# Kernel tuning notes

Hardware: AMD Instinct MI355X
Metric: run time of the kernel (lower is better)

## Reference

```python
import jax, jax.numpy as jnp
import numpy as np

BATCH = 256
NUM_PIXELS = 4096
NUM_LATENT = 8192
NUM_STEPS = 50
STEP_SIZE = 0.1
SPARSE_MULT = 0.1
EPS = 1e-8


def setup_inputs() -> dict:
    key = jax.random.key(0)
    k1, k2 = jax.random.split(key)
    input_tensor = jax.random.normal(k1, (BATCH, NUM_PIXELS), dtype=jnp.float32)
    w = jax.random.normal(k2, (NUM_PIXELS, NUM_LATENT), dtype=jnp.float32)
    # l2-normalize each dictionary element (column over pixel dim), as in dp.l2_normalize_weights
    w = w / (jnp.linalg.norm(w, axis=0, keepdims=True) + EPS)
    return {"input_tensor": input_tensor, "w": w}


def _threshold(u):
    # soft threshold with rectify_a=True: a = max(u - lambda, 0)
    return jnp.where(u > SPARSE_MULT, u - SPARSE_MULT, jnp.zeros_like(u))


def reference(input_tensor, w):
    # excitatory drive b = x @ w, constant over inference steps  [B, L]
    excitatory = jnp.matmul(input_tensor, w)
    # inhibitory Gram matrix G = w^T w - I  [L, L]
    gram = jnp.matmul(w.T, w) - jnp.eye(NUM_LATENT, dtype=w.dtype)

    def body(u, _):
        a = _threshold(u)
        du = excitatory - jnp.matmul(a, gram) - u
        return u + STEP_SIZE * du, None

    u0 = jnp.zeros((input_tensor.shape[0], NUM_LATENT), dtype=input_tensor.dtype)
    u_final, _ = jax.lax.scan(body, u0, None, length=NUM_STEPS - 1)
    a_final = _threshold(u_final)
    # reconstruction = a @ w^T  [B, P]
    return jnp.matmul(a_final, w.T)
```

## Files before the change

### kernel.cpp

```cpp
#include <hip/hip_runtime.h>
#include <stdint.h>
#include <math.h>

#define B_DIM 256
#define P_DIM 4096
#define L_DIM 8192
#define NSTEPS 50
#define STEP 0.1f
#define LAM 0.1f
#define FP8_ITERS 40
#define GSCALE 64.0f
#define ASCALE 16.0f
#define INV_SCALE (1.0f / (64.0f * 16.0f))

typedef __attribute__((ext_vector_type(8))) short bf16x8;
typedef __attribute__((ext_vector_type(4))) float f32x4;
typedef __attribute__((ext_vector_type(2))) long lgx2;

__device__ __forceinline__ unsigned short f2bf(float f) {
    union { float f; uint32_t u; } x; x.f = f;
    uint32_t r = (x.u + 0x7FFF + ((x.u >> 16) & 1)) >> 16;
    return (unsigned short)r;
}
__device__ __forceinline__ float bf2f(unsigned short h) {
    union { uint32_t u; float f; } x; x.u = (uint32_t)h << 16; return x.f;
}


__global__ void cast_x_kernel(const float* __restrict__ in, unsigned short* __restrict__ out, int n) {
    int i = (blockIdx.x * blockDim.x + threadIdx.x) * 4;
    if (i < n) {
        float4 v = *(const float4*)&in[i];
        ushort4 o;
        o.x = f2bf(v.x); o.y = f2bf(v.y); o.z = f2bf(v.z); o.w = f2bf(v.w);
        *(ushort4*)&out[i] = o;
    }
}

__global__ void cast_transpose_w(const float* __restrict__ w,
                                 unsigned short* __restrict__ w_bf,
                                 unsigned short* __restrict__ wT_bf) {
    __shared__ float tile[32][33];
    int c0 = blockIdx.x * 32;
    int r0 = blockIdx.y * 32;
    int tx = threadIdx.x, ty = threadIdx.y;
#pragma unroll
    for (int i = ty; i < 32; i += 8) {
        float v = w[(size_t)(r0 + i) * L_DIM + c0 + tx];
        tile[i][tx] = v;
        w_bf[(size_t)(r0 + i) * L_DIM + c0 + tx] = f2bf(v);
    }
    __syncthreads();
#pragma unroll
    for (int i = ty; i < 32; i += 8) {
        wT_bf[(size_t)(c0 + i) * P_DIM + r0 + tx] = f2bf(tile[tx][i]);
    }
}

__global__ void quantize_G(const unsigned short* __restrict__ G, unsigned char* __restrict__ Gf) {
    size_t i = ((size_t)blockIdx.x * 256 + threadIdx.x) * 8;
    bf16x8 v = *(const bf16x8*)&G[i];
    float f[8];
#pragma unroll
    for (int j = 0; j < 8; ++j) f[j] = bf2f((unsigned short)v[j]) * GSCALE;
    int q0 = __builtin_amdgcn_cvt_pk_fp8_f32(f[0], f[1], 0, false);
    q0 = __builtin_amdgcn_cvt_pk_fp8_f32(f[2], f[3], q0, true);
    int q1 = __builtin_amdgcn_cvt_pk_fp8_f32(f[4], f[5], 0, false);
    q1 = __builtin_amdgcn_cvt_pk_fp8_f32(f[6], f[7], q1, true);
    const int r = (int)(i & 127);
    size_t dst = (i & ~(size_t)127) + (size_t)((((r >> 6) & 1) << 6) + (((r >> 3) & 3) << 4) + (((r >> 5) & 1) << 3));
    *(int2*)(Gf + dst) = make_int2(q0, q1);
}

template <int BM, int BN, int BK, int WMC, int WNC, int EPI, int MM, int NN, int KK, int MAP>
__global__ __launch_bounds__(WMC * WNC * 64)
void gemm_pipe(const unsigned short* __restrict__ A,
               const unsigned short* __restrict__ Bt,
               float* __restrict__ Cf,
               float* __restrict__ uvec,
               unsigned short* __restrict__ aout,
               unsigned char* __restrict__ afp8) {
    constexpr int NWAVES = WMC * WNC;
    constexpr int WM = BM / WMC, WN = BN / WNC;
    constexpr int MF = WM / 16, NF = WN / 16;
    constexpr int ACH = BM / (8 * NWAVES);
    constexpr int BCH = BN / (8 * NWAVES);
    constexpr int LPS = ACH + BCH;
    constexpr int NT = KK / BK;
    static_assert(BK == 64, "swizzle hardcoded for BK=64");
    static_assert(ACH * 8 * NWAVES == BM && BCH * 8 * NWAVES == BN, "stage geometry");
    static_assert(NT % 4 == 0 && NT >= 8, "pipeline geometry");

    __shared__ __align__(16) unsigned short As[4][BM * BK];
    __shared__ __align__(16) unsigned short Bs[4][BN * BK];

    const int tid = threadIdx.x;
    const int w = tid >> 6;
    const int l = tid & 63;
    const int wr = w / WNC, wc = w % WNC;

    const int id = blockIdx.x;
    int bx, by;
    if constexpr (MAP == 0) {
        constexpr int PPX = (NN / BN) / 8;
        static_assert(MM / BM == 4 && (NN / BN) % 8 == 0, "panel map geometry");
        bx = (id & 7) * PPX + ((id >> 3) >> 2);
        by = (id >> 3) & 3;
    } else {
        constexpr int GY = MM / BM;
        by = id % GY;
        bx = id / GY;
    }
    const int row0 = by * BM;
    const int col0 = bx * BN;

    const int lrow = l >> 3;
    const int lcol = (((l & 7) ^ lrow) * 8);

    const unsigned short* gA = A + (size_t)(row0 + lrow) * KK + lcol;
    const unsigned short* gB = Bt + (size_t)(col0 + lrow) * KK + lcol;

    auto stage = [&](int buf, int k0) {
#pragma unroll
        for (int i = 0; i < ACH; ++i) {
            const int chunk = i * NWAVES + w;
            __builtin_amdgcn_global_load_lds(
                (const __attribute__((address_space(1))) void*)(gA + (size_t)chunk * 8 * KK + k0),
                (__attribute__((address_space(3))) void*)(&As[buf][chunk * 512]), 16, 0, 0);
        }
#pragma unroll
        for (int i = 0; i < BCH; ++i) {
            const int chunk = i * NWAVES + w;
            __builtin_amdgcn_global_load_lds(
                (const __attribute__((address_space(1))) void*)(gB + (size_t)chunk * 8 * KK + k0),
                (__attribute__((address_space(3))) void*)(&Bs[buf][chunk * 512]), 16, 0, 0);
        }
    };

    f32x4 acc[MF][NF] = {};

    auto compute = [&](int buf) {
#pragma unroll
        for (int kk = 0; kk < BK; kk += 32) {
            const int kslot = (kk >> 3) + (l >> 4);
            bf16x8 af[MF], bfr[NF];
#pragma unroll
            for (int mf = 0; mf < MF; ++mf) {
                const int arow = wr * WM + mf * 16 + (l & 15);
                af[mf] = *(const bf16x8*)&As[buf][arow * BK + ((kslot ^ (arow & 7)) << 3)];
            }
#pragma unroll
            for (int nf = 0; nf < NF; ++nf) {
                const int brow = wc * WN + nf * 16 + (l & 15);
                bfr[nf] = *(const bf16x8*)&Bs[buf][brow * BK + ((kslot ^ (brow & 7)) << 3)];
            }
#pragma unroll
            for (int mf = 0; mf < MF; ++mf)
#pragma unroll
                for (int nf = 0; nf < NF; ++nf)
                    acc[mf][nf] = __builtin_amdgcn_mfma_f32_16x16x32_bf16(
                        af[mf], bfr[nf], acc[mf][nf], 0, 0, 0);
        }
    };

#define PH(BUF, TT, WAITN, DOSTG)                                            \
    asm volatile("s_waitcnt vmcnt(%0)" ::"i"(WAITN) : "memory");             \
    __builtin_amdgcn_s_barrier();                                            \
    asm volatile("" ::: "memory");                                           \
    if (DOSTG) stage((BUF + 3) & 3, ((TT) + 3) * BK);                        \
    compute(BUF);

    stage(0, 0);
    stage(1, BK);
    stage(2, 2 * BK);
#pragma unroll 1
    for (int t = 0; t < NT - 4; t += 4) {
        PH(0, t + 0, 2 * LPS, true)
        PH(1, t + 1, 2 * LPS, true)
        PH(2, t + 2, 2 * LPS, true)
        PH(3, t + 3, 2 * LPS, true)
    }
    PH(0, NT - 4, 2 * LPS, true)
    PH(1, NT - 3, 2 * LPS, false)
    PH(2, NT - 2, LPS, false)
    PH(3, NT - 1, 0, false)
#undef PH

    const int er = (l >> 4) * 4;
    const int ec = l & 15;
#pragma unroll
    for (int mf = 0; mf < MF; ++mf) {
#pragma unroll
        for (int nf = 0; nf < NF; ++nf) {
#pragma unroll
            for (int j = 0; j < 4; ++j) {
                int gr = row0 + wr * WM + mf * 16 + er + j;
                int gc = col0 + wc * WN + nf * 16 + ec;
                size_t idx = (size_t)gr * NN + gc;
                float v = acc[mf][nf][j];
                if constexpr (EPI == 1) {
                    Cf[idx] = v;
                    float u0 = STEP * v;
                    uvec[idx] = u0;
                    float a = (u0 > LAM) ? (u0 - LAM) : 0.0f;
                    aout[idx] = f2bf(a);
                    float a16 = a * ASCALE;
                    int q = __builtin_amdgcn_cvt_pk_fp8_f32(a16, a16, 0, false);
                    const int r = gc & 127;
                    size_t fd = (size_t)gr * L_DIM + (size_t)(gc & ~127) +
                                (size_t)((((r >> 6) & 1) << 6) + (((r >> 3) & 3) << 4) + (((r >> 5) & 1) << 3) + (r & 7));
                    afp8[fd] = (unsigned char)(q & 0xff);
                } else {
                    Cf[idx] = v;
                }
            }
        }
    }
}

__global__ __launch_bounds__(512, 2)
void gemm_gram_sym(const unsigned short* __restrict__ A,
                   unsigned short* __restrict__ G) {
    constexpr int BM = 256, BN = 256, BK = 64;
    constexpr int WMC = 2, WNC = 4, NWAVES = 8;
    constexpr int WM = 128, WN = 64, MF = 8, NF = 4;
    constexpr int ACH = 4, BCH = 4, LPS = 8;
    constexpr int NT = P_DIM / BK;

    __shared__ __align__(16) unsigned short sh[4 * 256 * 64];
#define ASB(buf) (sh + (buf) * (256 * 64))
#define BSB(buf) (sh + (2 + (buf)) * (256 * 64))

    const int tid = threadIdx.x;
    const int w = tid >> 6;
    const int l = tid & 63;
    const int wr = w / WNC, wc = w % WNC;

    const int id = blockIdx.x;
    const int i = (int)((65.0f - sqrtf(4225.0f - 8.0f * (float)id)) * 0.5f);
    const int cum = i * (65 - i) / 2;
    const int j = i + (id - cum);
    const int by = i, bx = j;
    const int row0 = by * BM;
    const int col0 = bx * BN;

    const int lrow = l >> 3;
    const int lcol = (((l & 7) ^ lrow) * 8);

    const unsigned short* gA = A + (size_t)(row0 + lrow) * P_DIM + lcol;
    const unsigned short* gB = A + (size_t)(col0 + lrow) * P_DIM + lcol;

    auto stage = [&](int buf, int t) {
        const int k0 = t * BK;
#pragma unroll
        for (int c = 0; c < ACH; ++c) {
            const int chunk = c * NWAVES + w;
            __builtin_amdgcn_global_load_lds(
                (const __attribute__((address_space(1))) void*)(gA + (size_t)chunk * 8 * P_DIM + k0),
                (__attribute__((address_space(3))) void*)(ASB(buf) + chunk * 512), 16, 0, 0);
        }
#pragma unroll
        for (int c = 0; c < BCH; ++c) {
            const int chunk = c * NWAVES + w;
            __builtin_amdgcn_global_load_lds(
                (const __attribute__((address_space(1))) void*)(gB + (size_t)chunk * 8 * P_DIM + k0),
                (__attribute__((address_space(3))) void*)(BSB(buf) + chunk * 512), 16, 0, 0);
        }
    };

    f32x4 acc[MF][NF] = {};

    auto compute = [&](int buf) {
#pragma unroll
        for (int kk = 0; kk < BK; kk += 32) {
            const int kslot = (kk >> 3) + (l >> 4);
            bf16x8 af[MF], bfr[NF];
#pragma unroll
            for (int mf = 0; mf < MF; ++mf) {
                const int arow = wr * WM + mf * 16 + (l & 15);
                af[mf] = *(const bf16x8*)&ASB(buf)[arow * BK + ((kslot ^ (arow & 7)) << 3)];
            }
#pragma unroll
            for (int nf = 0; nf < NF; ++nf) {
                const int brow = wc * WN + nf * 16 + (l & 15);
                bfr[nf] = *(const bf16x8*)&BSB(buf)[brow * BK + ((kslot ^ (brow & 7)) << 3)];
            }
#pragma unroll
            for (int mf = 0; mf < MF; ++mf)
#pragma unroll
                for (int nf = 0; nf < NF; ++nf)
                    acc[mf][nf] = __builtin_amdgcn_mfma_f32_16x16x32_bf16(
                        af[mf], bfr[nf], acc[mf][nf], 0, 0, 0);
        }
    };

#define PH2(BUF, WAITN, DOSTG, TT)                                           \
    asm volatile("s_waitcnt vmcnt(%0)" ::"i"(WAITN) : "memory");             \
    __builtin_amdgcn_s_barrier();                                            \
    asm volatile("" ::: "memory");                                           \
    compute(BUF);                                                            \
    __builtin_amdgcn_s_barrier();                                            \
    asm volatile("" ::: "memory");                                           \
    if (DOSTG) stage(BUF, (TT) + 2);

    stage(0, 0);
    stage(1, 1);
#pragma unroll 1
    for (int t = 0; t < NT - 2; t += 2) {
        PH2(0, LPS, true, t)
        PH2(1, LPS, true, t + 1)
    }
    PH2(0, LPS, false, 0)
    PH2(1, 0, false, 0)
#undef PH2

    const int er = (l >> 4) * 4;
    const int ec = l & 15;

#pragma unroll
    for (int mf = 0; mf < MF; ++mf)
#pragma unroll
        for (int nf = 0; nf < NF; ++nf)
#pragma unroll
            for (int jj = 0; jj < 4; ++jj) {
                int gr = row0 + wr * WM + mf * 16 + er + jj;
                int gc = col0 + wc * WN + nf * 16 + ec;
                float v = acc[mf][nf][jj];
                if (gr == gc) v -= 1.0f;
                G[(size_t)gr * L_DIM + gc] = f2bf(v);
            }

    if (by != bx) {
        unsigned short* T = sh;
#pragma unroll 1
        for (int p = 0; p < 2; ++p) {
            __syncthreads();
            if ((wc >> 1) == p) {
#pragma unroll
                for (int mf = 0; mf < MF; ++mf)
#pragma unroll
                    for (int nf = 0; nf < NF; ++nf)
#pragma unroll
                        for (int jj = 0; jj < 4; ++jj) {
                            const int gr_l = wr * WM + mf * 16 + er + jj;
                            const int gc_l = (wc & 1) * 64 + nf * 16 + ec;
                            T[gc_l * 256 + (gr_l ^ ((gc_l & 7) << 2))] = f2bf(acc[mf][nf][jj]);
                        }
            }
            __syncthreads();
            const int rr = tid >> 6;
            const int cc = (tid & 63) * 4;
#pragma unroll
            for (int s = 0; s < 16; ++s) {
                const int r = s * 8 + rr;
                uint2 val = *(const uint2*)&T[r * 256 + (cc ^ ((r & 7) << 2))];
                *(uint2*)&G[(size_t)(col0 + p * 128 + r) * L_DIM + row0 + cc] = val;
            }
        }
    }
#undef ASB
#undef BSB
}

template <int BM, int BN, int WMC, int WNC, int EPI, int KROW, int KLOOP, int MAP>
__global__ __launch_bounds__(WMC * WNC * 64, 2)
void gemm2(const unsigned short* __restrict__ A,
           const unsigned short* __restrict__ Bt,
           unsigned short* __restrict__ Obf) {
    constexpr int NWAVES = WMC * WNC;
    constexpr int WM = BM / WMC, WN = BN / WNC;
    constexpr int MF = WM / 16, NF = WN / 16;
    constexpr int ACH = BM / (8 * NWAVES);
    constexpr int BCH = BN / (8 * NWAVES);
    constexpr int LPS = ACH + BCH;
    constexpr int BK = 64;
    constexpr int NT = KLOOP / BK;
    static_assert(ACH * 8 * NWAVES == BM && BCH * 8 * NWAVES == BN, "stage geometry");
    static_assert(NT % 2 == 0 && NT >= 4, "pipeline geometry");

    __shared__ __align__(16) unsigned short As[2][BM * BK];
    __shared__ __align__(16) unsigned short Bs[2][BN * BK];

    const int tid = threadIdx.x;
    const int w = tid >> 6;
    const int l = tid & 63;
    const int wr = w / WNC, wc = w % WNC;

    const int id = blockIdx.x;
    int bx, by, koff;
    size_t o_off;
    if constexpr (MAP == 2) {
        const int sb = id >> 4, wi = id & 15;
        by = (sb >> 3) * 4 + (wi >> 2);
        bx = (sb & 7) * 4 + (wi & 3);
        koff = 0;
        o_off = 0;
    } else {
        const int xcd = id & 7;
        by = (id >> 3) & 1;
        const int pp = id >> 4;
        const int slice = pp & 3;
        bx = xcd * 4 + (pp >> 2);
        koff = slice * KLOOP;
        o_off = (size_t)slice * B_DIM * L_DIM;
    }
    const int row0 = by * BM;
    const int col0 = bx * BN;

    const int lrow = l >> 3;
    const int lcol = (((l & 7) ^ lrow) * 8);

    const unsigned short* gA = A + (size_t)(row0 + lrow) * KROW + koff + lcol;
    const unsigned short* gB = Bt + (size_t)(col0 + lrow) * KROW + koff + lcol;

    auto stage = [&](int buf, int t) {
        const int k0 = t * BK;
#pragma unroll
        for (int i = 0; i < ACH; ++i) {
            const int chunk = i * NWAVES + w;
            __builtin_amdgcn_global_load_lds(
                (const __attribute__((address_space(1))) void*)(gA + (size_t)chunk * 8 * KROW + k0),
                (__attribute__((address_space(3))) void*)(&As[buf][chunk * 512]), 16, 0, 0);
        }
#pragma unroll
        for (int i = 0; i < BCH; ++i) {
            const int chunk = i * NWAVES + w;
            __builtin_amdgcn_global_load_lds(
                (const __attribute__((address_space(1))) void*)(gB + (size_t)chunk * 8 * KROW + k0),
                (__attribute__((address_space(3))) void*)(&Bs[buf][chunk * 512]), 16, 0, 0);
        }
    };

    f32x4 acc[MF][NF] = {};

    auto compute = [&](int buf) {
#pragma unroll
        for (int kk = 0; kk < BK; kk += 32) {
            const int kslot = (kk >> 3) + (l >> 4);
            bf16x8 af[MF], bfr[NF];
#pragma unroll
            for (int mf = 0; mf < MF; ++mf) {
                const int arow = wr * WM + mf * 16 + (l & 15);
                af[mf] = *(const bf16x8*)&As[buf][arow * BK + ((kslot ^ (arow & 7)) << 3)];
            }
#pragma unroll
            for (int nf = 0; nf < NF; ++nf) {
                const int brow = wc * WN + nf * 16 + (l & 15);
                bfr[nf] = *(const bf16x8*)&Bs[buf][brow * BK + ((kslot ^ (brow & 7)) << 3)];
            }
#pragma unroll
            for (int mf = 0; mf < MF; ++mf)
#pragma unroll
                for (int nf = 0; nf < NF; ++nf)
                    acc[mf][nf] = __builtin_amdgcn_mfma_f32_16x16x32_bf16(
                        af[mf], bfr[nf], acc[mf][nf], 0, 0, 0);
        }
    };

#define PH2(BUF, WAITN, DOSTG, TT)                                           \
    asm volatile("s_waitcnt vmcnt(%0)" ::"i"(WAITN) : "memory");             \
    __builtin_amdgcn_s_barrier();                                            \
    asm volatile("" ::: "memory");                                           \
    compute(BUF);                                                            \
    __builtin_amdgcn_s_barrier();                                            \
    asm volatile("" ::: "memory");                                           \
    if (DOSTG) stage(BUF, (TT) + 2);

    stage(0, 0);
    stage(1, 1);
#pragma unroll 1
    for (int t = 0; t < NT - 2; t += 2) {
        PH2(0, LPS, true, t)
        PH2(1, LPS, true, t + 1)
    }
    PH2(0, LPS, false, 0)
    PH2(1, 0, false, 0)
#undef PH2

    const int er = (l >> 4) * 4;
    const int ec = l & 15;
#pragma unroll
    for (int mf = 0; mf < MF; ++mf) {
#pragma unroll
        for (int nf = 0; nf < NF; ++nf) {
#pragma unroll
            for (int j = 0; j < 4; ++j) {
                int gr = row0 + wr * WM + mf * 16 + er + j;
                int gc = col0 + wc * WN + nf * 16 + ec;
                float v = acc[mf][nf][j];
                if constexpr (EPI == 0) {
                    if (gr == gc) v -= 1.0f;
                    Obf[(size_t)gr * L_DIM + gc] = f2bf(v);
                } else {
                    Obf[o_off + (size_t)gr * L_DIM + gc] = f2bf(v);
                }
            }
        }
    }
}

template <int BM, int BN, int WMC, int WNC>
__global__ __launch_bounds__(WMC * WNC * 64, 2)
void gemm_fp8(const unsigned char* __restrict__ A,
              const unsigned char* __restrict__ Bt,
              unsigned short* __restrict__ Obf) {
    constexpr int NWAVES = WMC * WNC;
    constexpr int WM = BM / WMC, WN = BN / WNC;
    constexpr int MF = WM / 16, NF = WN / 16;
    constexpr int BKB = 128;
    constexpr int ACH = BM / (8 * NWAVES);
    constexpr int BCH = BN / (8 * NWAVES);
    constexpr int LPS = ACH + BCH;
    constexpr int KLOOP = 2048;
    constexpr int NT = KLOOP / BKB;
    constexpr int KKB = L_DIM;
    static_assert(ACH * 8 * NWAVES == BM && BCH * 8 * NWAVES == BN, "stage geometry");

    __shared__ __align__(16) unsigned char As[2][BM * BKB];
    __shared__ __align__(16) unsigned char Bs[2][BN * BKB];

    const int tid = threadIdx.x;
    const int w = tid >> 6;
    const int l = tid & 63;
    const int wr = w / WNC, wc = w % WNC;

    const int id = blockIdx.x;
    const int xcd = id & 7;
    const int by = (id >> 3) & 1;
    const int pp = id >> 4;
    const int slice = pp & 3;
    const int bx = xcd * 4 + (pp >> 2);
    const int row0 = by * BM;
    const int col0 = bx * BN;
    const int koff = slice * KLOOP;

    const int lrow = l >> 3;
    const int lcol = (((l & 7) ^ lrow) << 4);

    const unsigned char* gA = A + (size_t)(row0 + lrow) * KKB + koff + lcol;
    const unsigned char* gB = Bt + (size_t)(col0 + lrow) * KKB + koff + lcol;

    auto stage = [&](int buf, int t) {
        const int k0 = t * BKB;
#pragma unroll
        for (int i = 0; i < ACH; ++i) {
            const int chunk = i * NWAVES + w;
            __builtin_amdgcn_global_load_lds(
                (const __attribute__((address_space(1))) void*)(gA + (size_t)chunk * 8 * KKB + k0),
                (__attribute__((address_space(3))) void*)(&As[buf][chunk * 1024]), 16, 0, 0);
        }
#pragma unroll
        for (int i = 0; i < BCH; ++i) {
            const int chunk = i * NWAVES + w;
            __builtin_amdgcn_global_load_lds(
                (const __attribute__((address_space(1))) void*)(gB + (size_t)chunk * 8 * KKB + k0),
                (__attribute__((address_space(3))) void*)(&Bs[buf][chunk * 1024]), 16, 0, 0);
        }
    };

    f32x4 acc[MF][NF] = {};

    auto compute = [&](int buf) {
#pragma unroll
        for (int kp = 0; kp < 2; ++kp) {
            const int c = kp * 4 + (l >> 4);
            lgx2 af[MF], bfr[NF];
#pragma unroll
            for (int mf = 0; mf < MF; ++mf) {
                const int arow = wr * WM + mf * 16 + (l & 15);
                af[mf] = *(const lgx2*)&As[buf][arow * BKB + ((c ^ (arow & 7)) << 4)];
            }
#pragma unroll
            for (int nf = 0; nf < NF; ++nf) {
                const int brow = wc * WN + nf * 16 + (l & 15);
                bfr[nf] = *(const lgx2*)&Bs[buf][brow * BKB + ((c ^ (brow & 7)) << 4)];
            }
#pragma unroll
            for (int mf = 0; mf < MF; ++mf)
#pragma unroll
                for (int nf = 0; nf < NF; ++nf) {
                    acc[mf][nf] = __builtin_amdgcn_mfma_f32_16x16x32_fp8_fp8(
                        af[mf][0], bfr[nf][0], acc[mf][nf], 0, 0, 0);
                    acc[mf][nf] = __builtin_amdgcn_mfma_f32_16x16x32_fp8_fp8(
                        af[mf][1], bfr[nf][1], acc[mf][nf], 0, 0, 0);
                }
        }
    };

#define PH2(BUF, WAITN, DOSTG, TT)                                           \
    asm volatile("s_waitcnt vmcnt(%0)" ::"i"(WAITN) : "memory");             \
    __builtin_amdgcn_s_barrier();                                            \
    asm volatile("" ::: "memory");                                           \
    compute(BUF);                                                            \
    __builtin_amdgcn_s_barrier();                                            \
    asm volatile("" ::: "memory");                                           \
    if (DOSTG) stage(BUF, (TT) + 2);

    stage(0, 0);
    stage(1, 1);
#pragma unroll 1
    for (int t = 0; t < NT - 2; t += 2) {
        PH2(0, LPS, true, t)
        PH2(1, LPS, true, t + 1)
    }
    PH2(0, LPS, false, 0)
    PH2(1, 0, false, 0)
#undef PH2

    const int er = (l >> 4) * 4;
    const int ec = l & 15;
    const size_t o_off = (size_t)slice * B_DIM * L_DIM;
#pragma unroll
    for (int mf = 0; mf < MF; ++mf)
#pragma unroll
        for (int nf = 0; nf < NF; ++nf)
#pragma unroll
            for (int j = 0; j < 4; ++j) {
                int gr = row0 + wr * WM + mf * 16 + er + j;
                int gc = col0 + wc * WN + nf * 16 + ec;
                Obf[o_off + (size_t)gr * L_DIM + gc] = f2bf(acc[mf][nf][j] * INV_SCALE);
            }
}

__global__ void reduce_iter(const unsigned short* __restrict__ P,
                            const float* __restrict__ bv,
                            float* __restrict__ uv,
                            unsigned short* __restrict__ an,
                            unsigned char* __restrict__ anf) {
    constexpr size_t SL = (size_t)B_DIM * L_DIM;
    size_t i = ((size_t)blockIdx.x * 256 + threadIdx.x) * 8;
    float s[8] = {};
#pragma unroll
    for (int sl = 0; sl < 4; ++sl) {
        ushort4 p0 = *(const ushort4*)&P[sl * SL + i];
        ushort4 p1 = *(const ushort4*)&P[sl * SL + i + 4];
        s[0] += bf2f(p0.x); s[1] += bf2f(p0.y); s[2] += bf2f(p0.z); s[3] += bf2f(p0.w);
        s[4] += bf2f(p1.x); s[5] += bf2f(p1.y); s[6] += bf2f(p1.z); s[7] += bf2f(p1.w);
    }
    float4 b0 = *(const float4*)&bv[i];
    float4 b1 = *(const float4*)&bv[i + 4];
    float4 u0 = *(const float4*)&uv[i];
    float4 u1 = *(const float4*)&uv[i + 4];
    float un[8];
    un[0] = 0.9f * u0.x + STEP * b0.x - STEP * s[0];
    un[1] = 0.9f * u0.y + STEP * b0.y - STEP * s[1];
    un[2] = 0.9f * u0.z + STEP * b0.z - STEP * s[2];
    un[3] = 0.9f * u0.w + STEP * b0.w - STEP * s[3];
    un[4] = 0.9f * u1.x + STEP * b1.x - STEP * s[4];
    un[5] = 0.9f * u1.y + STEP * b1.y - STEP * s[5];
    un[6] = 0.9f * u1.z + STEP * b1.z - STEP * s[6];
    un[7] = 0.9f * u1.w + STEP * b1.w - STEP * s[7];
    *(float4*)&uv[i] = make_float4(un[0], un[1], un[2], un[3]);
    *(float4*)&uv[i + 4] = make_float4(un[4], un[5], un[6], un[7]);
    float a[8];
#pragma unroll
    for (int j = 0; j < 8; ++j) a[j] = (un[j] > LAM) ? (un[j] - LAM) : 0.0f;
    ushort4 o0, o1;
    o0.x = f2bf(a[0]); o0.y = f2bf(a[1]); o0.z = f2bf(a[2]); o0.w = f2bf(a[3]);
    o1.x = f2bf(a[4]); o1.y = f2bf(a[5]); o1.z = f2bf(a[6]); o1.w = f2bf(a[7]);
    *(ushort4*)&an[i] = o0;
    *(ushort4*)&an[i + 4] = o1;
    int q0 = __builtin_amdgcn_cvt_pk_fp8_f32(a[0] * ASCALE, a[1] * ASCALE, 0, false);
    q0 = __builtin_amdgcn_cvt_pk_fp8_f32(a[2] * ASCALE, a[3] * ASCALE, q0, true);
    int q1 = __builtin_amdgcn_cvt_pk_fp8_f32(a[4] * ASCALE, a[5] * ASCALE, 0, false);
    q1 = __builtin_amdgcn_cvt_pk_fp8_f32(a[6] * ASCALE, a[7] * ASCALE, q1, true);
    const int r = (int)(i & 127);
    size_t dst = (i & ~(size_t)127) + (size_t)((((r >> 6) & 1) << 6) + (((r >> 3) & 3) << 4) + (((r >> 5) & 1) << 3));
    *(int2*)(anf + dst) = make_int2(q0, q1);
}

extern "C" void kernel_launch(void* const* d_in, const int* in_sizes, int n_in,
                              void* d_out, int out_size, void* d_ws, size_t ws_size,
                              hipStream_t stream) {
    (void)in_sizes; (void)n_in; (void)out_size; (void)ws_size;
    const float* x = (const float*)d_in[0];
    const float* w = (const float*)d_in[1];
    float* out = (float*)d_out;

    char* ws = (char*)d_ws;
    unsigned short* wT  = (unsigned short*)ws;
    unsigned char*  Gf  = (unsigned char*)ws;
    unsigned short* wbf = wT + (size_t)L_DIM * P_DIM;
    unsigned short* G   = wbf + (size_t)P_DIM * L_DIM;
    float* bv = (float*)(G + (size_t)L_DIM * L_DIM);
    float* uv = bv + (size_t)B_DIM * L_DIM;
    unsigned short* a0 = (unsigned short*)(uv + (size_t)B_DIM * L_DIM);
    unsigned short* a1 = a0 + (size_t)B_DIM * L_DIM;
    unsigned short* xbf = a1 + (size_t)B_DIM * L_DIM;
    unsigned char* a0f = (unsigned char*)(xbf + (size_t)B_DIM * P_DIM);
    unsigned char* a1f = a0f + (size_t)B_DIM * L_DIM;
    unsigned short* Ppart = (unsigned short*)(a1f + (size_t)B_DIM * L_DIM);

    cast_x_kernel<<<(B_DIM * P_DIM / 4 + 255) / 256, 256, 0, stream>>>(x, xbf, B_DIM * P_DIM);
    cast_transpose_w<<<dim3(L_DIM / 32, P_DIM / 32), dim3(32, 8), 0, stream>>>(w, wbf, wT);

    gemm_gram_sym<<<528, 512, 0, stream>>>(wT, G);

    gemm_pipe<64, 128, 64, 2, 4, 1, B_DIM, L_DIM, P_DIM, 0><<<256, 512, 0, stream>>>(
        xbf, wT, bv, uv, a0, a0f);

    quantize_G<<<(int)(((size_t)L_DIM * L_DIM / 8) / 256), 256, 0, stream>>>(G, Gf);

    unsigned short* ac = a0; unsigned short* an = a1;
    unsigned char* acf = a0f; unsigned char* anf = a1f;
    for (int it = 0; it < FP8_ITERS; ++it) {
        gemm_fp8<128, 256, 2, 4><<<256, 512, 0, stream>>>(acf, Gf, Ppart);
        reduce_iter<<<(B_DIM * L_DIM) / (256 * 8), 256, 0, stream>>>(Ppart, bv, uv, an, anf);
        unsigned short* t = ac; ac = an; an = t;
        unsigned char* tf = acf; acf = anf; anf = tf;
    }
    for (int it = 0; it < (NSTEPS - 2) - FP8_ITERS; ++it) {
        gemm2<128, 256, 2, 4, 4, L_DIM, 2048, 3><<<256, 512, 0, stream>>>(ac, G, Ppart);
        reduce_iter<<<(B_DIM * L_DIM) / (256 * 8), 256, 0, stream>>>(Ppart, bv, uv, an, anf);
        unsigned short* t = ac; ac = an; an = t;
        unsigned char* tf = acf; acf = anf; anf = tf;
    }

    gemm_pipe<64, 64, 64, 2, 4, 3, B_DIM, P_DIM, L_DIM, 0><<<256, 512, 0, stream>>>(
        ac, wbf, out, nullptr, nullptr, nullptr);
}
```

Measured before the change: 2.199 ms.

## Fuse split-K reduction and LCA update into GEMM epilogues via tile counters

Removes the separate reduce_iter launch after each iteration's GEMM. Each of the four split-K slice blocks for an output tile writes its bf16 partials, bumps a per-tile atomic counter and spin-waits until all four have arrived. Each block then reduces a quarter of the tile's rows and applies the u update, threshold and bf16/fp8 writes. This saves one launch and one kernel boundary per step, but relies on all 256 blocks being co-resident, which risks deadlock if occupancy falls short, and adds spin-wait latency.

Result: slower. 3.574 ms (+62.6%).

```diff
diff --git a/kernel.cpp b/kernel.cpp
--- a/kernel.cpp
+++ b/kernel.cpp
@@ -70,6 +70,77 @@
     const int r = (int)(i & 127);
     size_t dst = (i & ~(size_t)127) + (size_t)((((r >> 6) & 1) << 6) + (((r >> 3) & 3) << 4) + (((r >> 5) & 1) << 3));
     *(int2*)(Gf + dst) = make_int2(q0, q1);
+}
+
+__device__ __forceinline__ void fused_tile_reduce(
+    const unsigned short* __restrict__ P,
+    const float* __restrict__ bv, float* __restrict__ uv,
+    unsigned short* __restrict__ an, unsigned char* __restrict__ anf,
+    int* cnt_tile, int row0, int col0, int slice, int tid) {
+    __syncthreads();
+    if (tid == 0) {
+        __threadfence();
+        atomicAdd(cnt_tile, 1);
+        while (__hip_atomic_load(cnt_tile, __ATOMIC_ACQUIRE, __HIP_MEMORY_SCOPE_AGENT) < 4)
+            __builtin_amdgcn_s_sleep(8);
+        __threadfence();
+    }
+    __syncthreads();
+
+    const int rq = row0 + slice * 32 + (tid >> 4);
+    const int cq = col0 + (tid & 15) * 16;
+    const size_t base = (size_t)rq * L_DIM + cq;
+    constexpr size_t SL = (size_t)B_DIM * L_DIM;
+
+    float s[16];
+#pragma unroll
+    for (int j = 0; j < 16; ++j) s[j] = 0.0f;
+#pragma unroll
+    for (int sl = 0; sl < 4; ++sl) {
+        bf16x8 v0 = *(const bf16x8*)&P[sl * SL + base];
+        bf16x8 v1 = *(const bf16x8*)&P[sl * SL + base + 8];
+#pragma unroll
+        for (int j = 0; j < 8; ++j) {
+            s[j] += bf2f((unsigned short)v0[j]);
+            s[8 + j] += bf2f((unsigned short)v1[j]);
+        }
+    }
+    float un[16];
+#pragma unroll
+    for (int q = 0; q < 4; ++q) {
+        float4 b4 = *(const float4*)&bv[base + q * 4];
+        float4 u4 = *(const float4*)&uv[base + q * 4];
+        un[q * 4 + 0] = 0.9f * u4.x + STEP * b4.x - STEP * s[q * 4 + 0];
+        un[q * 4 + 1] = 0.9f * u4.y + STEP * b4.y - STEP * s[q * 4 + 1];
+        un[q * 4 + 2] = 0.9f * u4.z + STEP * b4.z - STEP * s[q * 4 + 2];
+        un[q * 4 + 3] = 0.9f * u4.w + STEP * b4.w - STEP * s[q * 4 + 3];
+        *(float4*)&uv[base + q * 4] =
+            make_float4(un[q * 4 + 0], un[q * 4 + 1], un[q * 4 + 2], un[q * 4 + 3]);
+    }
+    float a[16];
+#pragma unroll
+    for (int j = 0; j < 16; ++j) a[j] = (un[j] > LAM) ? (un[j] - LAM) : 0.0f;
+    bf16x8 oa0, oa1;
+#pragma unroll
+    for (int j = 0; j < 8; ++j) {
+        oa0[j] = (short)f2bf(a[j]);
+        oa1[j] = (short)f2bf(a[8 + j]);
+    }
+    *(bf16x8*)&an[base] = oa0;
+    *(bf16x8*)&an[base + 8] = oa1;
+#pragma unroll
+    for (int g = 0; g < 2; ++g) {
+        const float* ag = a + g * 8;
+        int q0 = __builtin_amdgcn_cvt_pk_fp8_f32(ag[0] * ASCALE, ag[1] * ASCALE, 0, false);
+        q0 = __builtin_amdgcn_cvt_pk_fp8_f32(ag[2] * ASCALE, ag[3] * ASCALE, q0, true);
+        int q1 = __builtin_amdgcn_cvt_pk_fp8_f32(ag[4] * ASCALE, ag[5] * ASCALE, 0, false);
+        q1 = __builtin_amdgcn_cvt_pk_fp8_f32(ag[6] * ASCALE, ag[7] * ASCALE, q1, true);
+        const int c = cq + g * 8;
+        const int r = c & 127;
+        size_t dst = (size_t)rq * L_DIM + (size_t)(c & ~127) +
+                     (size_t)((((r >> 6) & 1) << 6) + (((r >> 3) & 3) << 4) + (((r >> 5) & 1) << 3));
+        *(int2*)(anf + dst) = make_int2(q0, q1);
+    }
 }
 
 template <int BM, int BN, int BK, int WMC, int WNC, int EPI, int MM, int NN, int KK, int MAP>
@@ -362,21 +433,19 @@
 #undef BSB
 }
 
-template <int BM, int BN, int WMC, int WNC, int EPI, int KROW, int KLOOP, int MAP>
-__global__ __launch_bounds__(WMC * WNC * 64, 2)
-void gemm2(const unsigned short* __restrict__ A,
-           const unsigned short* __restrict__ Bt,
-           unsigned short* __restrict__ Obf) {
-    constexpr int NWAVES = WMC * WNC;
-    constexpr int WM = BM / WMC, WN = BN / WNC;
-    constexpr int MF = WM / 16, NF = WN / 16;
-    constexpr int ACH = BM / (8 * NWAVES);
-    constexpr int BCH = BN / (8 * NWAVES);
-    constexpr int LPS = ACH + BCH;
-    constexpr int BK = 64;
+__global__ __launch_bounds__(512, 2)
+void gemm_tail(const unsigned short* __restrict__ A,
+               const unsigned short* __restrict__ Bt,
+               unsigned short* __restrict__ Obf,
+               const float* __restrict__ bv, float* __restrict__ uv,
+               unsigned short* __restrict__ an, unsigned char* __restrict__ anf,
+               int* __restrict__ cnt) {
+    constexpr int BM = 128, BN = 256, BK = 64;
+    constexpr int WMC = 2, WNC = 4, NWAVES = 8;
+    constexpr int WM = 64, WN = 64, MF = 4, NF = 4;
+    constexpr int ACH = 2, BCH = 4, LPS = 6;
+    constexpr int KLOOP = 2048;
     constexpr int NT = KLOOP / BK;
-    static_assert(ACH * 8 * NWAVES == BM && BCH * 8 * NWAVES == BN, "stage geometry");
-    static_assert(NT % 2 == 0 && NT >= 4, "pipeline geometry");
 
     __shared__ __align__(16) unsigned short As[2][BM * BK];
     __shared__ __align__(16) unsigned short Bs[2][BN * BK];
@@ -387,31 +456,20 @@
     const int wr = w / WNC, wc = w % WNC;
 
     const int id = blockIdx.x;
-    int bx, by, koff;
-    size_t o_off;
-    if constexpr (MAP == 2) {
-        const int sb = id >> 4, wi = id & 15;
-        by = (sb >> 3) * 4 + (wi >> 2);
-        bx = (sb & 7) * 4 + (wi & 3);
-        koff = 0;
-        o_off = 0;
-    } else {
-        const int xcd = id & 7;
-        by = (id >> 3) & 1;
-        const int pp = id >> 4;
-        const int slice = pp & 3;
-        bx = xcd * 4 + (pp >> 2);
-        koff = slice * KLOOP;
-        o_off = (size_t)slice * B_DIM * L_DIM;
-    }
+    const int xcd = id & 7;
+    const int by = (id >> 3) & 1;
+    const int pp = id >> 4;
+    const int slice = pp & 3;
+    const int bx = xcd * 4 + (pp >> 2);
     const int row0 = by * BM;
     const int col0 = bx * BN;
+    const int koff = slice * KLOOP;
 
     const int lrow = l >> 3;
     const int lcol = (((l & 7) ^ lrow) * 8);
 
-    const unsigned short* gA = A + (size_t)(row0 + lrow) * KROW + koff + lcol;
-    const unsigned short* gB = Bt + (size_t)(col0 + lrow) * KROW + koff + lcol;
+    const unsigned short* gA = A + (size_t)(row0 + lrow) * L_DIM + koff + lcol;
+    const unsigned short* gB = Bt + (size_t)(col0 + lrow) * L_DIM + koff + lcol;
 
     auto stage = [&](int buf, int t) {
         const int k0 = t * BK;
@@ -419,14 +477,14 @@
         for (int i = 0; i < ACH; ++i) {
             const int chunk = i * NWAVES + w;
             __builtin_amdgcn_global_load_lds(
-                (const __attribute__((address_space(1))) void*)(gA + (size_t)chunk * 8 * KROW + k0),
+                (const __attribute__((address_space(1))) void*)(gA + (size_t)chunk * 8 * L_DIM + k0),
                 (__attribute__((address_space(3))) void*)(&As[buf][chunk * 512]), 16, 0, 0);
         }
 #pragma unroll
         for (int i = 0; i < BCH; ++i) {
             const int chunk = i * NWAVES + w;
             __builtin_amdgcn_global_load_lds(
-                (const __attribute__((address_space(1))) void*)(gB + (size_t)chunk * 8 * KROW + k0),
+                (const __attribute__((address_space(1))) void*)(gB + (size_t)chunk * 8 * L_DIM + k0),
                 (__attribute__((address_space(3))) void*)(&Bs[buf][chunk * 512]), 16, 0, 0);
         }
     };
@@ -479,31 +537,29 @@
 
     const int er = (l >> 4) * 4;
     const int ec = l & 15;
-#pragma unroll
-    for (int mf = 0; mf < MF; ++mf) {
-#pragma unroll
-        for (int nf = 0; nf < NF; ++nf) {
+    const size_t o_off = (size_t)slice * B_DIM * L_DIM;
+#pragma unroll
+    for (int mf = 0; mf < MF; ++mf)
+#pragma unroll
+        for (int nf = 0; nf < NF; ++nf)
 #pragma unroll
             for (int j = 0; j < 4; ++j) {
                 int gr = row0 + wr * WM + mf * 16 + er + j;
                 int gc = col0 + wc * WN + nf * 16 + ec;
-                float v = acc[mf][nf][j];
-                if constexpr (EPI == 0) {
-                    if (gr == gc) v -= 1.0f;
-                    Obf[(size_t)gr * L_DIM + gc] = f2bf(v);
-                } else {
-                    Obf[o_off + (size_t)gr * L_DIM + gc] = f2bf(v);
-                }
-            }
-        }
-    }
+                Obf[o_off + (size_t)gr * L_DIM + gc] = f2bf(acc[mf][nf][j]);
+            }
+
+    fused_tile_reduce(Obf, bv, uv, an, anf, cnt + ((by << 5) | bx), row0, col0, slice, tid);
 }
 
 template <int BM, int BN, int WMC, int WNC>
 __global__ __launch_bounds__(WMC * WNC * 64, 2)
 void gemm_fp8(const unsigned char* __restrict__ A,
               const unsigned char* __restrict__ Bt,
-              unsigned short* __restrict__ Obf) {
+              unsigned short* __restrict__ Obf,
+              const float* __restrict__ bv, float* __restrict__ uv,
+              unsigned short* __restrict__ an, unsigned char* __restrict__ anf,
+              int* __restrict__ cnt) {
     constexpr int NWAVES = WMC * WNC;
     constexpr int WM = BM / WMC, WN = BN / WNC;
     constexpr int MF = WM / 16, NF = WN / 16;
@@ -620,53 +676,8 @@
                 int gc = col0 + wc * WN + nf * 16 + ec;
                 Obf[o_off + (size_t)gr * L_DIM + gc] = f2bf(acc[mf][nf][j] * INV_SCALE);
             }
-}
-
-__global__ void reduce_iter(const unsigned short* __restrict__ P,
-                            const float* __restrict__ bv,
-                            float* __restrict__ uv,
-                            unsigned short* __restrict__ an,
-                            unsigned char* __restrict__ anf) {
-    constexpr size_t SL = (size_t)B_DIM * L_DIM;
-    size_t i = ((size_t)blockIdx.x * 256 + threadIdx.x) * 8;
-    float s[8] = {};
-#pragma unroll
-    for (int sl = 0; sl < 4; ++sl) {
-        ushort4 p0 = *(const ushort4*)&P[sl * SL + i];
-        ushort4 p1 = *(const ushort4*)&P[sl * SL + i + 4];
-        s[0] += bf2f(p0.x); s[1] += bf2f(p0.y); s[2] += bf2f(p0.z); s[3] += bf2f(p0.w);
-        s[4] += bf2f(p1.x); s[5] += bf2f(p1.y); s[6] += bf2f(p1.z); s[7] += bf2f(p1.w);
-    }
-    float4 b0 = *(const float4*)&bv[i];
-    float4 b1 = *(const float4*)&bv[i + 4];
-    float4 u0 = *(const float4*)&uv[i];
-    float4 u1 = *(const float4*)&uv[i + 4];
-    float un[8];
-    un[0] = 0.9f * u0.x + STEP * b0.x - STEP * s[0];
-    un[1] = 0.9f * u0.y + STEP * b0.y - STEP * s[1];
-    un[2] = 0.9f * u0.z + STEP * b0.z - STEP * s[2];
-    un[3] = 0.9f * u0.w + STEP * b0.w - STEP * s[3];
-    un[4] = 0.9f * u1.x + STEP * b1.x - STEP * s[4];
-    un[5] = 0.9f * u1.y + STEP * b1.y - STEP * s[5];
-    un[6] = 0.9f * u1.z + STEP * b1.z - STEP * s[6];
-    un[7] = 0.9f * u1.w + STEP * b1.w - STEP * s[7];
-    *(float4*)&uv[i] = make_float4(un[0], un[1], un[2], un[3]);
-    *(float4*)&uv[i + 4] = make_float4(un[4], un[5], un[6], un[7]);
-    float a[8];
-#pragma unroll
-    for (int j = 0; j < 8; ++j) a[j] = (un[j] > LAM) ? (un[j] - LAM) : 0.0f;
-    ushort4 o0, o1;
-    o0.x = f2bf(a[0]); o0.y = f2bf(a[1]); o0.z = f2bf(a[2]); o0.w = f2bf(a[3]);
-    o1.x = f2bf(a[4]); o1.y = f2bf(a[5]); o1.z = f2bf(a[6]); o1.w = f2bf(a[7]);
-    *(ushort4*)&an[i] = o0;
-    *(ushort4*)&an[i + 4] = o1;
-    int q0 = __builtin_amdgcn_cvt_pk_fp8_f32(a[0] * ASCALE, a[1] * ASCALE, 0, false);
-    q0 = __builtin_amdgcn_cvt_pk_fp8_f32(a[2] * ASCALE, a[3] * ASCALE, q0, true);
-    int q1 = __builtin_amdgcn_cvt_pk_fp8_f32(a[4] * ASCALE, a[5] * ASCALE, 0, false);
-    q1 = __builtin_amdgcn_cvt_pk_fp8_f32(a[6] * ASCALE, a[7] * ASCALE, q1, true);
-    const int r = (int)(i & 127);
-    size_t dst = (i & ~(size_t)127) + (size_t)((((r >> 6) & 1) << 6) + (((r >> 3) & 3) << 4) + (((r >> 5) & 1) << 3));
-    *(int2*)(anf + dst) = make_int2(q0, q1);
+
+    fused_tile_reduce(Obf, bv, uv, an, anf, cnt + ((by << 5) | bx), row0, col0, slice, tid);
 }
 
 extern "C" void kernel_launch(void* const* d_in, const int* in_sizes, int n_in,
@@ -690,6 +701,9 @@
     unsigned char* a0f = (unsigned char*)(xbf + (size_t)B_DIM * P_DIM);
     unsigned char* a1f = a0f + (size_t)B_DIM * L_DIM;
     unsigned short* Ppart = (unsigned short*)(a1f + (size_t)B_DIM * L_DIM);
+    int* cnt = (int*)(Ppart + (size_t)4 * B_DIM * L_DIM);
+
+    hipMemsetAsync(cnt, 0, (size_t)(NSTEPS - 2) * 64 * sizeof(int), stream);
 
     cast_x_kernel<<<(B_DIM * P_DIM / 4 + 255) / 256, 256, 0, stream>>>(x, xbf, B_DIM * P_DIM);
     cast_transpose_w<<<dim3(L_DIM / 32, P_DIM / 32), dim3(32, 8), 0, stream>>>(w, wbf, wT);
@@ -704,14 +718,14 @@
     unsigned short* ac = a0; unsigned short* an = a1;
     unsigned char* acf = a0f; unsigned char* anf = a1f;
     for (int it = 0; it < FP8_ITERS; ++it) {
-        gemm_fp8<128, 256, 2, 4><<<256, 512, 0, stream>>>(acf, Gf, Ppart);
-        reduce_iter<<<(B_DIM * L_DIM) / (256 * 8), 256, 0, stream>>>(Ppart, bv, uv, an, anf);
+        gemm_fp8<128, 256, 2, 4><<<256, 512, 0, stream>>>(
+            acf, Gf, Ppart, bv, uv, an, anf, cnt + it * 64);
         unsigned short* t = ac; ac = an; an = t;
         unsigned char* tf = acf; acf = anf; anf = tf;
     }
     for (int it = 0; it < (NSTEPS - 2) - FP8_ITERS; ++it) {
-        gemm2<128, 256, 2, 4, 4, L_DIM, 2048, 3><<<256, 512, 0, stream>>>(ac, G, Ppart);
-        reduce_iter<<<(B_DIM * L_DIM) / (256 * 8), 256, 0, stream>>>(Ppart, bv, uv, an, anf);
+        gemm_tail<<<256, 512, 0, stream>>>(
+            ac, G, Ppart, bv, uv, an, anf, cnt + (FP8_ITERS + it) * 64);
         unsigned short* t = ac; ac = an; an = t;
         unsigned char* tf = acf; acf = anf; anf = tf;
     }
```
